# Optimization experiments

Measured on AMD Instinct MI355X. Metric: run time of the kernel, lower is better.

The kernel has to match this reference:

```python
import jax, jax.numpy as jnp
import numpy as np

ALPHA = 32.0
RANK = 256
SCALE = ALPHA / RANK


def setup_inputs() -> dict:
    key = jax.random.key(0)
    k1, k2, k3, k4 = jax.random.split(key, 4)
    x = jax.random.normal(k1, (4, 2048, 4096), dtype=jnp.float32)
    A = jax.random.normal(k2, (256, 4096), dtype=jnp.float32)   # (rank, in)
    B = jax.random.normal(k3, (4096, 256), dtype=jnp.float32)   # (out, rank)
    d_A = jnp.ones((256,), dtype=jnp.float32)                    # init = ones (as in module)
    d_B = jax.random.normal(k4, (4096,), dtype=jnp.float32)      # perturbed for a nontrivial test
    return {"x": x, "A": A, "B": B, "d_A": d_A, "d_B": d_B}


def reference(x, A, B, d_A, d_B):
    # Effective weight: diag(d_B) @ B @ diag(d_A) @ A  -> (out, in)
    scaled_A = d_A[:, None] * A                 # (rank, in)
    BA = B @ scaled_A                            # (out, in)
    W_vera = d_B[:, None] * BA                   # (out, in)
    # out = x @ W_vera.T * scale  -> (..., out)
    return jnp.einsum('bsi,oi->bso', x, W_vera) * SCALE
```

## Files before the change

### kernel.cpp

```cpp
#include <hip/hip_runtime.h>
#include <hip/hip_bf16.h>


#define SCALE_F 0.125f
#define M_TOT 8192
#define K_IN 4096
#define RANK 256
#define N_OUT 4096
#define S_SPLIT 4
#define KC 1024

typedef __bf16 bf16_t;
typedef __bf16 bf16x8 __attribute__((ext_vector_type(8)));
typedef __bf16 bf16x4 __attribute__((ext_vector_type(4)));
typedef float f32x4 __attribute__((ext_vector_type(4)));

typedef __attribute__((address_space(3))) unsigned int lds_u32_t;
typedef const __attribute__((address_space(1))) unsigned int glob_u32_t;

__device__ __forceinline__ void async16(const void* g, void* l) {
    __builtin_amdgcn_global_load_lds((glob_u32_t*)g, (lds_u32_t*)l, 16, 0, 0);
}

__global__ __launch_bounds__(256) void conv_A(const float* __restrict__ A,
                                              const float* __restrict__ dA,
                                              bf16_t* __restrict__ Ab) {
    int idx = blockIdx.x * 256 + threadIdx.x;
    float4 v = ((const float4*)A)[idx];
    float s = dA[idx >> 10];
    bf16x4 o;
    o.x = (bf16_t)(v.x * s); o.y = (bf16_t)(v.y * s);
    o.z = (bf16_t)(v.z * s); o.w = (bf16_t)(v.w * s);
    ((bf16x4*)Ab)[idx] = o;
}

__global__ __launch_bounds__(256) void conv_B(const float* __restrict__ B,
                                              bf16_t* __restrict__ Bb) {
    int idx = blockIdx.x * 256 + threadIdx.x;
    float4 v = ((const float4*)B)[idx];
    bf16x4 o;
    o.x = (bf16_t)v.x; o.y = (bf16_t)v.y; o.z = (bf16_t)v.z; o.w = (bf16_t)v.w;
    ((bf16x4*)Bb)[idx] = o;
}

__global__ __launch_bounds__(256) void gemm1(const float* __restrict__ x,
                                             const bf16_t* __restrict__ Ab,
                                             bf16_t* __restrict__ part) {
    __shared__ float  sX[64 * 64];
    __shared__ bf16_t sA[128 * 64];
    const int tid = threadIdx.x;
    const int lane = tid & 63, wave = tid >> 6;
    const int wm = wave >> 1, wn = wave & 1;
    const int l15 = lane & 15, quad = lane >> 4;
    const int bm = blockIdx.x * 64;
    const int bn = blockIdx.y * 128;
    const int k0 = blockIdx.z * KC;

    f32x4 acc[2][4];
    const f32x4 zero = {0.f, 0.f, 0.f, 0.f};
    #pragma unroll
    for (int i = 0; i < 2; i++)
        #pragma unroll
        for (int j = 0; j < 4; j++) acc[i][j] = zero;

    for (int kt = 0; kt < KC; kt += 64) {
        #pragma unroll
        for (int c = 0; c < 4; c++) {
            int idx = c * 256 + tid;
            int m = idx >> 4, kc = (idx & 15) * 4;
            async16(&x[(size_t)(bm + m) * K_IN + k0 + kt + kc], &sX[idx * 4]);
        }
        #pragma unroll
        for (int c = 0; c < 4; c++) {
            int idx = c * 256 + tid;
            int n = idx >> 3, kc = (idx & 7) * 8;
            async16(&Ab[(size_t)(bn + n) * K_IN + k0 + kt + kc], &sA[idx * 8]);
        }
        __syncthreads();
        #pragma unroll
        for (int ks = 0; ks < 2; ks++) {
            bf16x8 af[2], bfr[4];
            #pragma unroll
            for (int i = 0; i < 2; i++) {
                const float* p = &sX[(wm * 32 + i * 16 + l15) * 64 + ks * 32 + quad * 8];
                f32x4 v0 = *(const f32x4*)p;
                f32x4 v1 = *(const f32x4*)(p + 4);
                bf16x8 t;
                t[0] = (bf16_t)v0[0]; t[1] = (bf16_t)v0[1];
                t[2] = (bf16_t)v0[2]; t[3] = (bf16_t)v0[3];
                t[4] = (bf16_t)v1[0]; t[5] = (bf16_t)v1[1];
                t[6] = (bf16_t)v1[2]; t[7] = (bf16_t)v1[3];
                af[i] = t;
            }
            #pragma unroll
            for (int j = 0; j < 4; j++)
                bfr[j] = *(const bf16x8*)&sA[(wn * 64 + j * 16 + l15) * 64 + ks * 32 + quad * 8];
            #pragma unroll
            for (int i = 0; i < 2; i++)
                #pragma unroll
                for (int j = 0; j < 4; j++)
                    acc[i][j] = __builtin_amdgcn_mfma_f32_16x16x32_bf16(af[i], bfr[j], acc[i][j], 0, 0, 0);
        }
        __syncthreads();
    }
    bf16_t* p = part + (size_t)blockIdx.z * M_TOT * RANK;
    #pragma unroll
    for (int i = 0; i < 2; i++) {
        #pragma unroll
        for (int j = 0; j < 4; j++) {
            int col = bn + wn * 64 + j * 16 + l15;
            #pragma unroll
            for (int r = 0; r < 4; r++) {
                int row = bm + wm * 32 + i * 16 + quad * 4 + r;
                p[(size_t)row * RANK + col] = (bf16_t)acc[i][j][r];
            }
        }
    }
}

__global__ __launch_bounds__(256) void reduce_t(const bf16_t* __restrict__ part,
                                                bf16_t* __restrict__ t) {
    int i = (blockIdx.x * 256 + threadIdx.x) * 8;
    float s[8] = {0.f, 0.f, 0.f, 0.f, 0.f, 0.f, 0.f, 0.f};
    #pragma unroll
    for (int z = 0; z < S_SPLIT; z++) {
        bf16x8 v = *(const bf16x8*)&part[(size_t)z * M_TOT * RANK + i];
        #pragma unroll
        for (int e = 0; e < 8; e++) s[e] += (float)v[e];
    }
    bf16x8 o;
    #pragma unroll
    for (int e = 0; e < 8; e++) o[e] = (bf16_t)s[e];
    *(bf16x8*)&t[i] = o;
}

__global__ __launch_bounds__(256) void gemm2(const bf16_t* __restrict__ t,
                                             const bf16_t* __restrict__ Bb,
                                             const float* __restrict__ dB,
                                             float* __restrict__ out) {
    __shared__ bf16_t sT[128 * 64];
    __shared__ bf16_t sB[64 * 64];
    const int tid = threadIdx.x;
    const int lane = tid & 63, wave = tid >> 6;
    const int wm = wave >> 1, wn = wave & 1;
    const int l15 = lane & 15, quad = lane >> 4;
    const int bm = blockIdx.x * 128;
    const int bn = blockIdx.y * 64;

    f32x4 acc[4][2];
    const f32x4 zero = {0.f, 0.f, 0.f, 0.f};
    #pragma unroll
    for (int i = 0; i < 4; i++)
        #pragma unroll
        for (int j = 0; j < 2; j++) acc[i][j] = zero;

    for (int kt = 0; kt < RANK; kt += 64) {
        #pragma unroll
        for (int c = 0; c < 4; c++) {
            int idx = c * 256 + tid;
            int m = idx >> 3, kc = (idx & 7) * 8;
            async16(&t[(size_t)(bm + m) * RANK + kt + kc], &sT[idx * 8]);
        }
        #pragma unroll
        for (int c = 0; c < 2; c++) {
            int idx = c * 256 + tid;
            int n = idx >> 3, kc = (idx & 7) * 8;
            async16(&Bb[(size_t)(bn + n) * RANK + kt + kc], &sB[idx * 8]);
        }
        __syncthreads();
        #pragma unroll
        for (int ks = 0; ks < 2; ks++) {
            bf16x8 af[4], bfr[2];
            #pragma unroll
            for (int i = 0; i < 4; i++)
                af[i] = *(const bf16x8*)&sT[(wm * 64 + i * 16 + l15) * 64 + ks * 32 + quad * 8];
            #pragma unroll
            for (int j = 0; j < 2; j++)
                bfr[j] = *(const bf16x8*)&sB[(wn * 32 + j * 16 + l15) * 64 + ks * 32 + quad * 8];
            #pragma unroll
            for (int i = 0; i < 4; i++)
                #pragma unroll
                for (int j = 0; j < 2; j++)
                    acc[i][j] = __builtin_amdgcn_mfma_f32_16x16x32_bf16(af[i], bfr[j], acc[i][j], 0, 0, 0);
        }
        __syncthreads();
    }
    #pragma unroll
    for (int j = 0; j < 2; j++) {
        int col = bn + wn * 32 + j * 16 + l15;
        float db = dB[col] * SCALE_F;
        #pragma unroll
        for (int i = 0; i < 4; i++) {
            #pragma unroll
            for (int r = 0; r < 4; r++) {
                int row = bm + wm * 64 + i * 16 + quad * 4 + r;
                out[(size_t)row * N_OUT + col] = db * acc[i][j][r];
            }
        }
    }
}

extern "C" void kernel_launch(void* const* d_in, const int* in_sizes, int n_in,
                              void* d_out, int out_size, void* d_ws, size_t ws_size,
                              hipStream_t stream) {
    const float* x  = (const float*)d_in[0];
    const float* A  = (const float*)d_in[1];
    const float* B  = (const float*)d_in[2];
    const float* dA = (const float*)d_in[3];
    const float* dB = (const float*)d_in[4];
    float* out = (float*)d_out;

    char* ws = (char*)d_ws;
    bf16_t* Ab   = (bf16_t*)ws;
    bf16_t* Bb   = (bf16_t*)(ws + (1u << 21));
    bf16_t* tt   = (bf16_t*)(ws + (1u << 22));
    bf16_t* part = (bf16_t*)(ws + (1u << 23));

    conv_A<<<1024, 256, 0, stream>>>(A, dA, Ab);
    conv_B<<<1024, 256, 0, stream>>>(B, Bb);
    gemm1<<<dim3(128, 2, S_SPLIT), 256, 0, stream>>>(x, Ab, part);
    reduce_t<<<1024, 256, 0, stream>>>(part, tt);
    gemm2<<<dim3(64, 64), 256, 0, stream>>>(tt, Bb, dB, out);
}
```

Baseline: 314.6 us.

## Double-buffer both GEMMs with swizzled LDS and convert x to bf16 before staging

gemm1 now loads x through registers, converts it to bf16 once, and stores it into an XOR-swizzled, double-buffered LDS tile. The next tile's loads are issued before computing on the current one, so memory latency overlaps MFMA work and x takes half the LDS space. gemm2 gets the same double buffering and swizzle, and its output tile grows to 128x128 with a 4x4 accumulator per wave, which halves the grid and the re-reads of the rank-256 intermediate. The cost is more registers and LDS per block, which may lower occupancy, and each block now does a register-staged global load for x before the compute step.

```diff
diff --git a/kernel.cpp b/kernel.cpp
--- a/kernel.cpp
+++ b/kernel.cpp
@@ -46,8 +46,8 @@
 __global__ __launch_bounds__(256) void gemm1(const float* __restrict__ x,
                                              const bf16_t* __restrict__ Ab,
                                              bf16_t* __restrict__ part) {
-    __shared__ float  sX[64 * 64];
-    __shared__ bf16_t sA[128 * 64];
+    __shared__ bf16_t sX[2][64 * 64];
+    __shared__ bf16_t sA[2][128 * 64];
     const int tid = threadIdx.x;
     const int lane = tid & 63, wave = tid >> 6;
     const int wm = wave >> 1, wn = wave & 1;
@@ -63,47 +63,82 @@
         #pragma unroll
         for (int j = 0; j < 4; j++) acc[i][j] = zero;
 
-    for (int kt = 0; kt < KC; kt += 64) {
+    f32x4 xr[2][2];
+
+    auto issue_x = [&](int kk) {
+        #pragma unroll
+        for (int c = 0; c < 2; c++) {
+            int idx = c * 256 + tid;
+            int row = idx >> 3, sl = idx & 7;
+            const float* sp = &x[(size_t)(bm + row) * K_IN + kk + sl * 8];
+            xr[c][0] = *(const f32x4*)sp;
+            xr[c][1] = *(const f32x4*)(sp + 4);
+        }
+    };
+    auto stage_a = [&](int b, int kk) {
         #pragma unroll
         for (int c = 0; c < 4; c++) {
             int idx = c * 256 + tid;
-            int m = idx >> 4, kc = (idx & 15) * 4;
-            async16(&x[(size_t)(bm + m) * K_IN + k0 + kt + kc], &sX[idx * 4]);
-        }
-        #pragma unroll
-        for (int c = 0; c < 4; c++) {
-            int idx = c * 256 + tid;
-            int n = idx >> 3, kc = (idx & 7) * 8;
-            async16(&Ab[(size_t)(bn + n) * K_IN + k0 + kt + kc], &sA[idx * 8]);
-        }
-        __syncthreads();
+            int row = idx >> 3, sl = idx & 7;
+            async16(&Ab[(size_t)(bn + row) * K_IN + kk + ((sl ^ (row & 7)) << 3)],
+                    &sA[b][idx * 8]);
+        }
+    };
+    auto write_x = [&](int b) {
+        #pragma unroll
+        for (int c = 0; c < 2; c++) {
+            int idx = c * 256 + tid;
+            int row = idx >> 3, sl = idx & 7;
+            bf16x8 o;
+            #pragma unroll
+            for (int e = 0; e < 4; e++) {
+                o[e]     = (bf16_t)xr[c][0][e];
+                o[e + 4] = (bf16_t)xr[c][1][e];
+            }
+            *(bf16x8*)&sX[b][row * 64 + ((sl ^ (row & 7)) << 3)] = o;
+        }
+    };
+    auto compute = [&](int b) {
         #pragma unroll
         for (int ks = 0; ks < 2; ks++) {
             bf16x8 af[2], bfr[4];
             #pragma unroll
             for (int i = 0; i < 2; i++) {
-                const float* p = &sX[(wm * 32 + i * 16 + l15) * 64 + ks * 32 + quad * 8];
-                f32x4 v0 = *(const f32x4*)p;
-                f32x4 v1 = *(const f32x4*)(p + 4);
-                bf16x8 t;
-                t[0] = (bf16_t)v0[0]; t[1] = (bf16_t)v0[1];
-                t[2] = (bf16_t)v0[2]; t[3] = (bf16_t)v0[3];
-                t[4] = (bf16_t)v1[0]; t[5] = (bf16_t)v1[1];
-                t[6] = (bf16_t)v1[2]; t[7] = (bf16_t)v1[3];
-                af[i] = t;
-            }
-            #pragma unroll
-            for (int j = 0; j < 4; j++)
-                bfr[j] = *(const bf16x8*)&sA[(wn * 64 + j * 16 + l15) * 64 + ks * 32 + quad * 8];
+                int row = wm * 32 + i * 16 + l15;
+                af[i] = *(const bf16x8*)&sX[b][row * 64 + ((((ks << 2) | quad) ^ (row & 7)) << 3)];
+            }
+            #pragma unroll
+            for (int j = 0; j < 4; j++) {
+                int row = wn * 64 + j * 16 + l15;
+                bfr[j] = *(const bf16x8*)&sA[b][row * 64 + ((((ks << 2) | quad) ^ (row & 7)) << 3)];
+            }
             #pragma unroll
             for (int i = 0; i < 2; i++)
                 #pragma unroll
                 for (int j = 0; j < 4; j++)
                     acc[i][j] = __builtin_amdgcn_mfma_f32_16x16x32_bf16(af[i], bfr[j], acc[i][j], 0, 0, 0);
         }
+    };
+
+    issue_x(k0);
+    stage_a(0, k0);
+    write_x(0);
+    __syncthreads();
+
+    int cur = 0;
+    for (int it = 1; it < KC / 64; ++it) {
+        const int nxt = cur ^ 1;
+        const int kk = k0 + it * 64;
+        issue_x(kk);
+        stage_a(nxt, kk);
+        compute(cur);
+        write_x(nxt);
         __syncthreads();
-    }
-    bf16_t* p = part + (size_t)blockIdx.z * M_TOT * RANK;
+        cur = nxt;
+    }
+    compute(cur);
+
+    bf16_t* p = part + (size_t)blockIdx.z * (M_TOT * RANK);
     #pragma unroll
     for (int i = 0; i < 2; i++) {
         #pragma unroll
@@ -138,56 +173,75 @@
                                              const bf16_t* __restrict__ Bb,
                                              const float* __restrict__ dB,
                                              float* __restrict__ out) {
-    __shared__ bf16_t sT[128 * 64];
-    __shared__ bf16_t sB[64 * 64];
+    __shared__ bf16_t sT[2][128 * 64];
+    __shared__ bf16_t sB[2][128 * 64];
     const int tid = threadIdx.x;
     const int lane = tid & 63, wave = tid >> 6;
     const int wm = wave >> 1, wn = wave & 1;
     const int l15 = lane & 15, quad = lane >> 4;
     const int bm = blockIdx.x * 128;
-    const int bn = blockIdx.y * 64;
-
-    f32x4 acc[4][2];
+    const int bn = blockIdx.y * 128;
+
+    f32x4 acc[4][4];
     const f32x4 zero = {0.f, 0.f, 0.f, 0.f};
     #pragma unroll
     for (int i = 0; i < 4; i++)
         #pragma unroll
-        for (int j = 0; j < 2; j++) acc[i][j] = zero;
-
-    for (int kt = 0; kt < RANK; kt += 64) {
+        for (int j = 0; j < 4; j++) acc[i][j] = zero;
+
+    auto stage = [&](int b, int kt) {
         #pragma unroll
         for (int c = 0; c < 4; c++) {
             int idx = c * 256 + tid;
-            int m = idx >> 3, kc = (idx & 7) * 8;
-            async16(&t[(size_t)(bm + m) * RANK + kt + kc], &sT[idx * 8]);
-        }
-        #pragma unroll
-        for (int c = 0; c < 2; c++) {
-            int idx = c * 256 + tid;
-            int n = idx >> 3, kc = (idx & 7) * 8;
-            async16(&Bb[(size_t)(bn + n) * RANK + kt + kc], &sB[idx * 8]);
-        }
-        __syncthreads();
+            int row = idx >> 3, sl = idx & 7;
+            async16(&t[(size_t)(bm + row) * RANK + kt + ((sl ^ (row & 7)) << 3)],
+                    &sT[b][idx * 8]);
+        }
+        #pragma unroll
+        for (int c = 0; c < 4; c++) {
+            int idx = c * 256 + tid;
+            int row = idx >> 3, sl = idx & 7;
+            async16(&Bb[(size_t)(bn + row) * RANK + kt + ((sl ^ (row & 7)) << 3)],
+                    &sB[b][idx * 8]);
+        }
+    };
+    auto compute = [&](int b) {
         #pragma unroll
         for (int ks = 0; ks < 2; ks++) {
-            bf16x8 af[4], bfr[2];
-            #pragma unroll
-            for (int i = 0; i < 4; i++)
-                af[i] = *(const bf16x8*)&sT[(wm * 64 + i * 16 + l15) * 64 + ks * 32 + quad * 8];
-            #pragma unroll
-            for (int j = 0; j < 2; j++)
-                bfr[j] = *(const bf16x8*)&sB[(wn * 32 + j * 16 + l15) * 64 + ks * 32 + quad * 8];
+            bf16x8 af[4], bfr[4];
+            #pragma unroll
+            for (int i = 0; i < 4; i++) {
+                int row = wm * 64 + i * 16 + l15;
+                af[i] = *(const bf16x8*)&sT[b][row * 64 + ((((ks << 2) | quad) ^ (row & 7)) << 3)];
+            }
+            #pragma unroll
+            for (int j = 0; j < 4; j++) {
+                int row = wn * 64 + j * 16 + l15;
+                bfr[j] = *(const bf16x8*)&sB[b][row * 64 + ((((ks << 2) | quad) ^ (row & 7)) << 3)];
+            }
             #pragma unroll
             for (int i = 0; i < 4; i++)
                 #pragma unroll
-                for (int j = 0; j < 2; j++)
+                for (int j = 0; j < 4; j++)
                     acc[i][j] = __builtin_amdgcn_mfma_f32_16x16x32_bf16(af[i], bfr[j], acc[i][j], 0, 0, 0);
         }
+    };
+
+    stage(0, 0);
+    __syncthreads();
+    int cur = 0;
+    #pragma unroll
+    for (int it = 1; it < RANK / 64; ++it) {
+        stage(cur ^ 1, it * 64);
+        compute(cur);
         __syncthreads();
-    }
-    #pragma unroll
-    for (int j = 0; j < 2; j++) {
-        int col = bn + wn * 32 + j * 16 + l15;
+        cur ^= 1;
+    }
+    compute(cur);
+
+    #pragma unroll
+    for (int j = 0; j < 4; j++) {
+        int col = bn + wn * 64 + j * 16 + l15;
         float db = dB[col] * SCALE_F;
         #pragma unroll
         for (int i = 0; i < 4; i++) {
@@ -220,5 +274,5 @@
     conv_B<<<1024, 256, 0, stream>>>(B, Bb);
     gemm1<<<dim3(128, 2, S_SPLIT), 256, 0, stream>>>(x, Ab, part);
     reduce_t<<<1024, 256, 0, stream>>>(part, tt);
-    gemm2<<<dim3(64, 64), 256, 0, stream>>>(tt, Bb, dB, out);
-}
+    gemm2<<<dim3(64, 32), 256, 0, stream>>>(tt, Bb, dB, out);
+}
```

Measured after the change: 328.6 us. 1.04x slower.
